# Performance work log

Hardware: AMD Instinct MI355X
Metric: run time of the kernel (lower is better)

The kernel has to match this reference:

```python
import jax, jax.numpy as jnp
import numpy as np

ALPHA = 0.2  # LeakyReLU negative slope
NEG_INF = -9e15


def setup_inputs() -> dict:
    key = jax.random.key(0)
    k1, k2, k3, k4 = jax.random.split(key, 4)
    N, F_in, F_out = 8192, 256, 64
    h = jax.random.normal(k1, (N, F_in), dtype=jnp.float32)
    adj = jax.random.randint(k2, (N, N), 0, 2, dtype=jnp.int32)
    # xavier-uniform-style scaling for params
    W = jax.random.normal(k3, (F_in, F_out), dtype=jnp.float32) * (1.0 / np.sqrt(F_in))
    a = jax.random.normal(k4, (2 * F_out, 1), dtype=jnp.float32) * (1.0 / np.sqrt(F_out))
    return {"h": h, "adj": adj, "W": W, "a": a}


def reference(h, adj, W, a):
    # Wh: [N, F_out]
    Wh = h @ W
    F_out = W.shape[1]
    a1 = a[:F_out, 0]   # attends to source (row i)
    a2 = a[F_out:, 0]   # attends to target (row j)
    f1 = Wh @ a1        # [N]
    f2 = Wh @ a2        # [N]
    # e[i, j] = leakyrelu(Wh_i . a1 + Wh_j . a2)  == original repeat/cat math
    e = jax.nn.leaky_relu(f1[:, None] + f2[None, :], negative_slope=ALPHA)
    attention = jnp.where(adj > 0, e, NEG_INF)
    attention = jax.nn.softmax(attention, axis=1)
    # dropout omitted (eval / deterministic reference)
    h_prime = attention @ Wh  # [N, F_out]
    return jax.nn.elu(h_prime)
```

## Files before the change

kernel.cpp:

```cpp
#include <hip/hip_runtime.h>
#include <hip/hip_bf16.h>
#include <stdint.h>

#define N 8192
#define FIN 256
#define FOUT 64

typedef __attribute__((ext_vector_type(8))) short s8v;
typedef __attribute__((ext_vector_type(4))) float f4v;

__device__ __forceinline__ uint32_t f2bf(float f) {
  uint32_t u = __float_as_uint(f);
  return (u + 0x7FFFu + ((u >> 16) & 1u)) >> 16;
}

__global__ __launch_bounds__(64) void gat_prep(
    const float* __restrict__ h, const float* __restrict__ W,
    const float* __restrict__ a,
    float* __restrict__ f1, float* __restrict__ f2,
    uint16_t* __restrict__ whT)
{
  const int c = threadIdx.x;
  const int i0 = blockIdx.x * 8;
  float acc[8] = {0.f, 0.f, 0.f, 0.f, 0.f, 0.f, 0.f, 0.f};
  #pragma unroll 4
  for (int k = 0; k < FIN; ++k) {
    float wv = W[k * FOUT + c];
    #pragma unroll
    for (int r = 0; r < 8; ++r)
      acc[r] += h[(size_t)(i0 + r) * FIN + k] * wv;
  }
  uint32_t b[8];
  #pragma unroll
  for (int r = 0; r < 8; ++r) b[r] = f2bf(acc[r]);
  int4 pk;
  pk.x = (int)(b[0] | (b[1] << 16));
  pk.y = (int)(b[2] | (b[3] << 16));
  pk.z = (int)(b[4] | (b[5] << 16));
  pk.w = (int)(b[6] | (b[7] << 16));
  *(int4*)(whT + (size_t)c * N + i0) = pk;

  const float a1 = a[c], a2 = a[FOUT + c];
  #pragma unroll
  for (int r = 0; r < 8; ++r) {
    float v1 = acc[r] * a1;
    float v2 = acc[r] * a2;
    #pragma unroll
    for (int m = 32; m > 0; m >>= 1) {
      v1 += __shfl_xor(v1, m, 64);
      v2 += __shfl_xor(v2, m, 64);
    }
    if (c == 0) { f1[i0 + r] = v1; f2[i0 + r] = v2; }
  }
}

__global__ __launch_bounds__(256) void gat_main(
    const int* __restrict__ adj, const float* __restrict__ f1,
    const float* __restrict__ f2, const uint16_t* __restrict__ whT,
    float* __restrict__ out)
{
  __shared__ __align__(16) uint16_t w_lds[16][72];
  __shared__ __align__(16) uint16_t v_lds[64][72];
  __shared__ float den_lds[16][16];
  __shared__ float den_fin[16];

  const int t = threadIdx.x;
  const int i0 = blockIdx.x * 16;
  const int i_loc = t >> 4;
  const int jsel  = t & 15;
  const int cc    = t >> 2;
  const int joff  = (t & 3) * 16;

  const float f1v = f1[i0 + i_loc];
  const int* adj_row = adj + (size_t)(i0 + i_loc) * N + jsel * 4;
  const float* f2p = f2 + jsel * 4;
  const uint16_t* vrow = whT + (size_t)cc * N + joff;

  int4   adjv = *(const int4*)(adj_row);
  float4 f2v  = *(const float4*)(f2p);
  int4   wa   = *(const int4*)(vrow);
  int4   wb   = *(const int4*)(vrow + 8);

  const int lane = t & 63;
  const int wv   = t >> 6;
  const int arow = lane & 15;
  const int aq   = lane >> 4;
  const int c0   = wv * 16;

  f4v acc = {0.f, 0.f, 0.f, 0.f};
  float den_acc = 0.f;

  for (int jc = 0; jc < N / 64; ++jc) {
    float e0 = f1v + f2v.x; e0 = fmaxf(e0, 0.2f * e0);
    float e1 = f1v + f2v.y; e1 = fmaxf(e1, 0.2f * e1);
    float e2 = f1v + f2v.z; e2 = fmaxf(e2, 0.2f * e2);
    float e3 = f1v + f2v.w; e3 = fmaxf(e3, 0.2f * e3);
    float w0 = (adjv.x > 0) ? __expf(e0) : 0.f;
    float w1 = (adjv.y > 0) ? __expf(e1) : 0.f;
    float w2 = (adjv.z > 0) ? __expf(e2) : 0.f;
    float w3 = (adjv.w > 0) ? __expf(e3) : 0.f;
    uint32_t u0 = f2bf(w0), u1 = f2bf(w1), u2 = f2bf(w2), u3 = f2bf(w3);
    den_acc += __uint_as_float(u0 << 16) + __uint_as_float(u1 << 16)
             + __uint_as_float(u2 << 16) + __uint_as_float(u3 << 16);
    *(uint2*)&w_lds[i_loc][jsel * 4] = make_uint2(u0 | (u1 << 16), u2 | (u3 << 16));
    *(int4*)&v_lds[cc][joff]     = wa;
    *(int4*)&v_lds[cc][joff + 8] = wb;
    if (jc + 1 < N / 64) {
      int jn = (jc + 1) * 64;
      adjv = *(const int4*)(adj_row + jn);
      f2v  = *(const float4*)(f2p + jn);
      wa   = *(const int4*)(vrow + jn);
      wb   = *(const int4*)(vrow + jn + 8);
    }
    __syncthreads();
    s8v a0 = *(const s8v*)&w_lds[arow][aq * 8];
    s8v a1 = *(const s8v*)&w_lds[arow][32 + aq * 8];
    s8v b0 = *(const s8v*)&v_lds[c0 + arow][aq * 8];
    s8v b1 = *(const s8v*)&v_lds[c0 + arow][32 + aq * 8];
    acc = __builtin_amdgcn_mfma_f32_16x16x32_bf16(a0, b0, acc, 0, 0, 0);
    acc = __builtin_amdgcn_mfma_f32_16x16x32_bf16(a1, b1, acc, 0, 0, 0);
    __syncthreads();
  }

  den_lds[i_loc][jsel] = den_acc;
  __syncthreads();
  if (t < 16) {
    float s = 0.f;
    #pragma unroll
    for (int u = 0; u < 16; ++u) s += den_lds[t][u];
    den_fin[t] = s;
  }
  __syncthreads();

  #pragma unroll
  for (int r = 0; r < 4; ++r) {
    int i_row = aq * 4 + r;
    float hp = acc[r] / den_fin[i_row];
    float o = (hp > 0.f) ? hp : (__expf(hp) - 1.f);
    out[(size_t)(i0 + i_row) * FOUT + c0 + arow] = o;
  }
}

extern "C" void kernel_launch(void* const* d_in, const int* in_sizes, int n_in,
                              void* d_out, int out_size, void* d_ws, size_t ws_size,
                              hipStream_t stream) {
  const float* h   = (const float*)d_in[0];
  const int*   adj = (const int*)d_in[1];
  const float* W   = (const float*)d_in[2];
  const float* a   = (const float*)d_in[3];
  float* out = (float*)d_out;

  float* f1 = (float*)d_ws;
  float* f2 = f1 + N;
  uint16_t* whT = (uint16_t*)(f2 + N);

  gat_prep<<<N / 8, 64, 0, stream>>>(h, W, a, f1, f2, whT);
  gat_main<<<N / 16, 256, 0, stream>>>(adj, f1, f2, whT, out);
}
```

Before: 449.0 us.

## Split attention over four column quarters per wave, drop LDS, add combine kernel

The main kernel is restructured so that each wave owns a 16-row group and one quarter of the columns. It builds the MFMA A fragments directly in registers from adj and f2, and loads the B fragments of Wh^T straight from global memory, so the LDS staging and the two barriers per iteration are gone. Partial numerators and denominators go to workspace, and a new combine kernel sums the four quarters and applies the normalization and ELU. This raises parallelism and removes synchronization overhead. In exchange it adds extra global traffic for the partials, a third launch, and uncoalesced reads of Wh^T that each wave repeats.

```diff
diff --git a/kernel.cpp b/kernel.cpp
--- a/kernel.cpp
+++ b/kernel.cpp
@@ -54,91 +54,113 @@
   }
 }
 
-__global__ __launch_bounds__(256) void gat_main(
+__device__ __forceinline__ s8v make_afrag(float f1v, const int* __restrict__ ap,
+                                          const float* __restrict__ fp, float& den) {
+  int4 c0 = *(const int4*)ap;
+  int4 c1 = *(const int4*)(ap + 4);
+  float4 g0 = *(const float4*)fp;
+  float4 g1 = *(const float4*)(fp + 4);
+  float e0 = f1v + g0.x; e0 = fmaxf(e0, 0.2f * e0); float w0 = (c0.x > 0) ? __expf(e0) : 0.f;
+  float e1 = f1v + g0.y; e1 = fmaxf(e1, 0.2f * e1); float w1 = (c0.y > 0) ? __expf(e1) : 0.f;
+  float e2 = f1v + g0.z; e2 = fmaxf(e2, 0.2f * e2); float w2 = (c0.z > 0) ? __expf(e2) : 0.f;
+  float e3 = f1v + g0.w; e3 = fmaxf(e3, 0.2f * e3); float w3 = (c0.w > 0) ? __expf(e3) : 0.f;
+  float e4 = f1v + g1.x; e4 = fmaxf(e4, 0.2f * e4); float w4 = (c1.x > 0) ? __expf(e4) : 0.f;
+  float e5 = f1v + g1.y; e5 = fmaxf(e5, 0.2f * e5); float w5 = (c1.y > 0) ? __expf(e5) : 0.f;
+  float e6 = f1v + g1.z; e6 = fmaxf(e6, 0.2f * e6); float w6 = (c1.z > 0) ? __expf(e6) : 0.f;
+  float e7 = f1v + g1.w; e7 = fmaxf(e7, 0.2f * e7); float w7 = (c1.w > 0) ? __expf(e7) : 0.f;
+  uint32_t b0 = f2bf(w0), b1 = f2bf(w1), b2 = f2bf(w2), b3 = f2bf(w3);
+  uint32_t b4 = f2bf(w4), b5 = f2bf(w5), b6 = f2bf(w6), b7 = f2bf(w7);
+  den += __uint_as_float(b0 << 16) + __uint_as_float(b1 << 16)
+       + __uint_as_float(b2 << 16) + __uint_as_float(b3 << 16)
+       + __uint_as_float(b4 << 16) + __uint_as_float(b5 << 16)
+       + __uint_as_float(b6 << 16) + __uint_as_float(b7 << 16);
+  union { s8v v; uint32_t u[4]; } r;
+  r.u[0] = b0 | (b1 << 16);
+  r.u[1] = b2 | (b3 << 16);
+  r.u[2] = b4 | (b5 << 16);
+  r.u[3] = b6 | (b7 << 16);
+  return r.v;
+}
+
+__global__ __launch_bounds__(256) void gat_main2(
     const int* __restrict__ adj, const float* __restrict__ f1,
     const float* __restrict__ f2, const uint16_t* __restrict__ whT,
+    float* __restrict__ pnum, float* __restrict__ pden)
+{
+  const int t = threadIdx.x;
+  const int wave = t >> 6;
+  const int lane = t & 63;
+  const int task = blockIdx.x * 4 + wave;
+  const int group = task >> 2;
+  const int quarter = task & 3;
+  const int i0 = group * 16;
+  const int jb = quarter * (N / 4);
+  const int m  = lane & 15;
+  const int kg = lane >> 4;
+
+  const float f1v = f1[i0 + m];
+  const int*      ap  = adj + (size_t)(i0 + m) * N + jb + kg * 8;
+  const float*    fp  = f2 + jb + kg * 8;
+  const uint16_t* bp0 = whT + (size_t)m * N + jb + kg * 8;
+
+  f4v acc0 = {0.f, 0.f, 0.f, 0.f};
+  f4v acc1 = acc0, acc2 = acc0, acc3 = acc0;
+  float den = 0.f;
+
+  #pragma unroll 2
+  for (int jc = 0; jc < (N / 4) / 64; ++jc) {
+    const int j0 = jc * 64;
+    s8v a0 = make_afrag(f1v, ap + j0,      fp + j0,      den);
+    s8v a1 = make_afrag(f1v, ap + j0 + 32, fp + j0 + 32, den);
+    const uint16_t* bp = bp0 + j0;
+    s8v b00 = *(const s8v*)(bp);
+    s8v b01 = *(const s8v*)(bp + 32);
+    s8v b10 = *(const s8v*)(bp + 16 * N);
+    s8v b11 = *(const s8v*)(bp + 16 * N + 32);
+    s8v b20 = *(const s8v*)(bp + 32 * N);
+    s8v b21 = *(const s8v*)(bp + 32 * N + 32);
+    s8v b30 = *(const s8v*)(bp + 48 * N);
+    s8v b31 = *(const s8v*)(bp + 48 * N + 32);
+    acc0 = __builtin_amdgcn_mfma_f32_16x16x32_bf16(a0, b00, acc0, 0, 0, 0);
+    acc0 = __builtin_amdgcn_mfma_f32_16x16x32_bf16(a1, b01, acc0, 0, 0, 0);
+    acc1 = __builtin_amdgcn_mfma_f32_16x16x32_bf16(a0, b10, acc1, 0, 0, 0);
+    acc1 = __builtin_amdgcn_mfma_f32_16x16x32_bf16(a1, b11, acc1, 0, 0, 0);
+    acc2 = __builtin_amdgcn_mfma_f32_16x16x32_bf16(a0, b20, acc2, 0, 0, 0);
+    acc2 = __builtin_amdgcn_mfma_f32_16x16x32_bf16(a1, b21, acc2, 0, 0, 0);
+    acc3 = __builtin_amdgcn_mfma_f32_16x16x32_bf16(a0, b30, acc3, 0, 0, 0);
+    acc3 = __builtin_amdgcn_mfma_f32_16x16x32_bf16(a1, b31, acc3, 0, 0, 0);
+  }
+
+  den += __shfl_xor(den, 16, 64);
+  den += __shfl_xor(den, 32, 64);
+
+  float* np = pnum + (size_t)task * (16 * 64);
+  #pragma unroll
+  for (int r = 0; r < 4; ++r) {
+    int row = kg * 4 + r;
+    np[row * 64 +      m] = acc0[r];
+    np[row * 64 + 16 + m] = acc1[r];
+    np[row * 64 + 32 + m] = acc2[r];
+    np[row * 64 + 48 + m] = acc3[r];
+  }
+  if (lane < 16) pden[task * 16 + m] = den;
+}
+
+__global__ __launch_bounds__(256) void gat_combine(
+    const float* __restrict__ pnum, const float* __restrict__ pden,
     float* __restrict__ out)
 {
-  __shared__ __align__(16) uint16_t w_lds[16][72];
-  __shared__ __align__(16) uint16_t v_lds[64][72];
-  __shared__ float den_lds[16][16];
-  __shared__ float den_fin[16];
-
-  const int t = threadIdx.x;
-  const int i0 = blockIdx.x * 16;
-  const int i_loc = t >> 4;
-  const int jsel  = t & 15;
-  const int cc    = t >> 2;
-  const int joff  = (t & 3) * 16;
-
-  const float f1v = f1[i0 + i_loc];
-  const int* adj_row = adj + (size_t)(i0 + i_loc) * N + jsel * 4;
-  const float* f2p = f2 + jsel * 4;
-  const uint16_t* vrow = whT + (size_t)cc * N + joff;
-
-  int4   adjv = *(const int4*)(adj_row);
-  float4 f2v  = *(const float4*)(f2p);
-  int4   wa   = *(const int4*)(vrow);
-  int4   wb   = *(const int4*)(vrow + 8);
-
-  const int lane = t & 63;
-  const int wv   = t >> 6;
-  const int arow = lane & 15;
-  const int aq   = lane >> 4;
-  const int c0   = wv * 16;
-
-  f4v acc = {0.f, 0.f, 0.f, 0.f};
-  float den_acc = 0.f;
-
-  for (int jc = 0; jc < N / 64; ++jc) {
-    float e0 = f1v + f2v.x; e0 = fmaxf(e0, 0.2f * e0);
-    float e1 = f1v + f2v.y; e1 = fmaxf(e1, 0.2f * e1);
-    float e2 = f1v + f2v.z; e2 = fmaxf(e2, 0.2f * e2);
-    float e3 = f1v + f2v.w; e3 = fmaxf(e3, 0.2f * e3);
-    float w0 = (adjv.x > 0) ? __expf(e0) : 0.f;
-    float w1 = (adjv.y > 0) ? __expf(e1) : 0.f;
-    float w2 = (adjv.z > 0) ? __expf(e2) : 0.f;
-    float w3 = (adjv.w > 0) ? __expf(e3) : 0.f;
-    uint32_t u0 = f2bf(w0), u1 = f2bf(w1), u2 = f2bf(w2), u3 = f2bf(w3);
-    den_acc += __uint_as_float(u0 << 16) + __uint_as_float(u1 << 16)
-             + __uint_as_float(u2 << 16) + __uint_as_float(u3 << 16);
-    *(uint2*)&w_lds[i_loc][jsel * 4] = make_uint2(u0 | (u1 << 16), u2 | (u3 << 16));
-    *(int4*)&v_lds[cc][joff]     = wa;
-    *(int4*)&v_lds[cc][joff + 8] = wb;
-    if (jc + 1 < N / 64) {
-      int jn = (jc + 1) * 64;
-      adjv = *(const int4*)(adj_row + jn);
-      f2v  = *(const float4*)(f2p + jn);
-      wa   = *(const int4*)(vrow + jn);
-      wb   = *(const int4*)(vrow + jn + 8);
-    }
-    __syncthreads();
-    s8v a0 = *(const s8v*)&w_lds[arow][aq * 8];
-    s8v a1 = *(const s8v*)&w_lds[arow][32 + aq * 8];
-    s8v b0 = *(const s8v*)&v_lds[c0 + arow][aq * 8];
-    s8v b1 = *(const s8v*)&v_lds[c0 + arow][32 + aq * 8];
-    acc = __builtin_amdgcn_mfma_f32_16x16x32_bf16(a0, b0, acc, 0, 0, 0);
-    acc = __builtin_amdgcn_mfma_f32_16x16x32_bf16(a1, b1, acc, 0, 0, 0);
-    __syncthreads();
-  }
-
-  den_lds[i_loc][jsel] = den_acc;
-  __syncthreads();
-  if (t < 16) {
-    float s = 0.f;
-    #pragma unroll
-    for (int u = 0; u < 16; ++u) s += den_lds[t][u];
-    den_fin[t] = s;
-  }
-  __syncthreads();
-
-  #pragma unroll
-  for (int r = 0; r < 4; ++r) {
-    int i_row = aq * 4 + r;
-    float hp = acc[r] / den_fin[i_row];
-    float o = (hp > 0.f) ? hp : (__expf(hp) - 1.f);
-    out[(size_t)(i0 + i_row) * FOUT + c0 + arow] = o;
-  }
+  const int idx = blockIdx.x * 256 + threadIdx.x;
+  const int i = idx >> 6;
+  const int c = idx & 63;
+  const int g = i >> 4;
+  const int r = i & 15;
+  const size_t base = (size_t)g * 4 * 1024 + (size_t)r * 64 + c;
+  float num = pnum[base] + pnum[base + 1024] + pnum[base + 2048] + pnum[base + 3072];
+  const int db = g * 64 + r;
+  float den = pden[db] + pden[db + 16] + pden[db + 32] + pden[db + 48];
+  float hp = num / den;
+  out[idx] = (hp > 0.f) ? hp : (__expf(hp) - 1.f);
 }
 
 extern "C" void kernel_launch(void* const* d_in, const int* in_sizes, int n_in,
@@ -153,7 +175,10 @@
   float* f1 = (float*)d_ws;
   float* f2 = f1 + N;
   uint16_t* whT = (uint16_t*)(f2 + N);
+  float* pnum = (float*)(whT + (size_t)FOUT * N);
+  float* pden = pnum + (size_t)2048 * 16 * 64;
 
   gat_prep<<<N / 8, 64, 0, stream>>>(h, W, a, f1, f2, whT);
-  gat_main<<<N / 16, 256, 0, stream>>>(adj, f1, f2, whT, out);
+  gat_main2<<<512, 256, 0, stream>>>(adj, f1, f2, whT, pnum, pden);
+  gat_combine<<<(N * FOUT) / 256, 256, 0, stream>>>(pnum, pden, out);
 }
```

Measured after the change: 436.9 us. 2.7% less time.
